# Kernel tuning notes

Hardware: AMD Instinct MI355X
Metric: run time of the kernel (lower is better)

Reference implementation:

```python
import math
import jax, jax.numpy as jnp
import numpy as np

NHEADS = 4
EPS = 1e-8


def setup_inputs() -> dict:
    key = jax.random.key(0)
    ks = jax.random.split(key, 5)
    B, C, D, H, W = 2, 64, 16, 16, 16
    dk = C // NHEADS
    x = jax.random.normal(ks[0], (B, C, D, H, W), dtype=jnp.float32)
    # xavier-uniform bound for a [nheads, dmodel, dk] tensor (torch fan_in=dmodel*dk, fan_out=nheads*dk)
    bound = math.sqrt(6.0 / (C * dk + NHEADS * dk))
    def xav(k):
        return jax.random.uniform(k, (NHEADS, C, dk), dtype=jnp.float32, minval=-bound, maxval=bound)
    return {"x": x, "wq": xav(ks[1]), "wk": xav(ks[2]), "wv": xav(ks[3]), "wo": xav(ks[4])}


def _cosine_attn(q, k, v):
    # q,k: (B,H,N,dk), v: (B,H,N,dv)
    qn = q / (jnp.linalg.norm(q, axis=-1, keepdims=True) + EPS)
    kn = k / (jnp.linalg.norm(k, axis=-1, keepdims=True) + EPS)
    scores = jnp.einsum('bhnd,bhmd->bhnm', qn, kn)  # (B,H,N,N)
    weights = jax.nn.softmax(scores, axis=-1)
    return jnp.einsum('bhnm,bhmv->bhnv', weights, v)


def reference(x, wq, wk, wv, wo):
    B, C, D, H, W = x.shape
    heads = NHEADS
    dv = C // heads
    # rearrange (B,C,D,H,W) -> (B, N, C) with N = D*H*W
    t = x.reshape(B, C, D * H * W).transpose(0, 2, 1)
    # per-kind 1/sqrt(fan_in) scaling (normalize_weight is identity here)
    wq_s = wq / math.sqrt(C)
    wk_s = wk / math.sqrt(C)
    wv_s = wv / math.sqrt(C)
    wo_s = wo / math.sqrt(heads * dv)
    q = jnp.einsum('bnc,hck->bhnk', t, wq_s)
    k = jnp.einsum('bnc,hck->bhnk', t, wk_s)
    v = jnp.einsum('bnc,hcv->bhnv', t, wv_s)
    o = _cosine_attn(q, k, v)  # (B,H,N,dv)
    y = jnp.einsum('bhnv,hcv->bnc', o, wo_s)
    return y.transpose(0, 2, 1).reshape(B, C, D, H, W)
```

## Files before the change

kernel.cpp:

```cpp
#include <hip/hip_runtime.h>
#include <math.h>

#define NHEADS 4
#define DKK 16
#define CC 64
#define BB 2
#define NN 4096
#define NBH 8
#define EPSF 1e-8f
#define KSPLIT 8
#define TILES 32
#define LOG2E 1.44269504088896340736f

typedef __attribute__((ext_vector_type(8))) short bf8;
typedef __attribute__((ext_vector_type(4))) float f4;

union Frag { bf8 v; struct { uint2 lo, hi; } p; uint4 q; };

__device__ __forceinline__ unsigned short f2bf(float f) {
    union { float f; unsigned int u; } v; v.f = f;
    unsigned int r = v.u + 0x7FFFu + ((v.u >> 16) & 1u);
    return (unsigned short)(r >> 16);
}
__device__ __forceinline__ float bf2f(unsigned short h) {
    union { unsigned int u; float f; } v; v.u = ((unsigned int)h) << 16;
    return v.f;
}

__global__ __launch_bounds__(256) void proj_kernel(
    const float* __restrict__ x, const float* __restrict__ wq,
    const float* __restrict__ wk, const float* __restrict__ wv,
    unsigned short* __restrict__ QP, unsigned short* __restrict__ KP,
    unsigned short* __restrict__ VP)
{
    __shared__ float sW[3 * CC * DKK];
    const int bh = blockIdx.x >> 6;
    const int n0 = (blockIdx.x & 63) * 64;
    const int b  = bh >> 2;
    const int h  = bh & 3;

    const int hbase = h * CC * DKK;
    for (int i = threadIdx.x; i < CC * DKK; i += 256) {
        sW[i]                = wq[hbase + i] * 0.125f;
        sW[CC * DKK + i]     = wk[hbase + i] * 0.125f;
        sW[2 * CC * DKK + i] = wv[hbase + i] * 0.125f;
    }
    __syncthreads();

    const int lane = threadIdx.x & 63;
    const int wave = threadIdx.x >> 6;
    const int n  = n0 + wave * 16 + (lane & 15);
    const int cq = lane >> 4;

    float aq[DKK] = {}, ak[DKK] = {}, av[DKK] = {};
    const float* xb = x + (size_t)b * CC * NN + n;
    for (int cc = 0; cc < 16; ++cc) {
        const int c = cq * 16 + cc;
        const float xv = xb[(size_t)c * NN];
        const float4* q4 = (const float4*)(sW + c * DKK);
        const float4* k4 = (const float4*)(sW + CC * DKK + c * DKK);
        const float4* v4 = (const float4*)(sW + 2 * CC * DKK + c * DKK);
        #pragma unroll
        for (int j = 0; j < 4; ++j) {
            float4 a = q4[j];
            aq[4*j+0] += xv * a.x; aq[4*j+1] += xv * a.y;
            aq[4*j+2] += xv * a.z; aq[4*j+3] += xv * a.w;
            float4 bk = k4[j];
            ak[4*j+0] += xv * bk.x; ak[4*j+1] += xv * bk.y;
            ak[4*j+2] += xv * bk.z; ak[4*j+3] += xv * bk.w;
            float4 cv = v4[j];
            av[4*j+0] += xv * cv.x; av[4*j+1] += xv * cv.y;
            av[4*j+2] += xv * cv.z; av[4*j+3] += xv * cv.w;
        }
    }
    #pragma unroll
    for (int i = 0; i < DKK; ++i) {
        aq[i] += __shfl_xor(aq[i], 16); aq[i] += __shfl_xor(aq[i], 32);
        ak[i] += __shfl_xor(ak[i], 16); ak[i] += __shfl_xor(ak[i], 32);
        av[i] += __shfl_xor(av[i], 16); av[i] += __shfl_xor(av[i], 32);
    }

    float sq = 0.f, sk = 0.f;
    #pragma unroll
    for (int i = 0; i < DKK; ++i) { sq += aq[i]*aq[i]; sk += ak[i]*ak[i]; }
    const float rq = LOG2E / (sqrtf(sq) + EPSF);
    const float rk = 1.0f / (sqrtf(sk) + EPSF);

    if (cq == 0) {
        __attribute__((aligned(16))) unsigned short qp[16];
        #pragma unroll
        for (int i = 0; i < DKK; ++i) qp[i] = f2bf(aq[i] * rq);
        const size_t base = ((size_t)bh * NN + n) * 16;
        ((uint4*)(QP + base))[0] = ((const uint4*)qp)[0];
        ((uint4*)(QP + base))[1] = ((const uint4*)qp)[1];
    } else if (cq == 1) {
        __attribute__((aligned(16))) unsigned short kp[16];
        #pragma unroll
        for (int i = 0; i < DKK; ++i) kp[i] = f2bf(ak[i] * rk);
        const size_t base = ((size_t)bh * NN + n) * 16;
        ((uint4*)(KP + base))[0] = ((const uint4*)kp)[0];
        ((uint4*)(KP + base))[1] = ((const uint4*)kp)[1];
    } else {
        const size_t vbase = (((size_t)bh * DKK) * 256 + (n >> 4)) * 32
                             + ((n >> 2) & 3) * 8 + (n & 3) + (cq == 2 ? 0 : 4);
        #pragma unroll
        for (int i = 0; i < DKK; ++i) {
            const float vv = av[i];
            const unsigned short hv = f2bf(vv);
            VP[vbase + (size_t)i * 256 * 32] =
                (cq == 2) ? hv : f2bf(vv - bf2f(hv));
        }
    }
}

__device__ __forceinline__ void attn_tile(
    const uint2 khi, const Frag& vc,
    const Frag* qh_, f4* oC, float* l_)
{
    const f4 zero = {0.f, 0.f, 0.f, 0.f};
    Frag kA;
    kA.p.lo = khi; kA.p.hi = make_uint2(0u, 0u);

    #pragma unroll
    for (int f = 0; f < 4; ++f) {
        f4 s = __builtin_amdgcn_mfma_f32_16x16x32_bf16(kA.v, qh_[f].v, zero, 0, 0, 0);

        const float p0 = __builtin_amdgcn_exp2f(s[0]);
        const float p1 = __builtin_amdgcn_exp2f(s[1]);
        const float p2 = __builtin_amdgcn_exp2f(s[2]);
        const float p3 = __builtin_amdgcn_exp2f(s[3]);
        l_[f] += (p0 + p1) + (p2 + p3);

        unsigned int u0, u1;
        asm("v_cvt_pk_bf16_f32 %0, %1, %2" : "=v"(u0) : "v"(p0), "v"(p1));
        asm("v_cvt_pk_bf16_f32 %0, %1, %2" : "=v"(u1) : "v"(p2), "v"(p3));
        Frag pB;
        pB.p.lo = make_uint2(u0, u1); pB.p.hi = pB.p.lo;

        oC[f] = __builtin_amdgcn_mfma_f32_16x16x32_bf16(vc.v, pB.v, oC[f], 0, 0, 0);
    }
}

__global__ __launch_bounds__(512, 4) void attn_kernel(
    const unsigned short* __restrict__ QP, const unsigned short* __restrict__ KP,
    const unsigned short* __restrict__ VP, float* __restrict__ O2T)
{
    const int bh    = blockIdx.x & 7;
    const int qg    = blockIdx.x >> 3;
    const int split = threadIdx.x >> 6;
    const int lane  = threadIdx.x & 63;
    const int g = lane >> 4;
    const int r = lane & 15;

    Frag qh_[4];
    #pragma unroll
    for (int f = 0; f < 4; ++f) {
        const uint2 qv = *(const uint2*)(QP + ((size_t)bh * NN + qg * 64 + f * 16 + r) * 16 + g * 4);
        qh_[f].p.lo = qv; qh_[f].p.hi = qv;
    }

    const int key0 = split * (NN / KSPLIT);
    const unsigned short* kp_p = KP + ((size_t)bh * NN + key0 + r) * 16 + g * 4;
    const unsigned short* vp_p = VP + (((size_t)bh * DKK + r) * 256 + (key0 >> 4)) * 32 + g * 8;

    f4 oC[4] = {{0.f,0.f,0.f,0.f},{0.f,0.f,0.f,0.f},{0.f,0.f,0.f,0.f},{0.f,0.f,0.f,0.f}};
    float l_[4] = {0.f, 0.f, 0.f, 0.f};

    uint2 k0 = *(const uint2*)kp_p;
    Frag  v0; v0.q = *(const uint4*)vp_p;
    uint2 k1 = *(const uint2*)(kp_p + 256);
    Frag  v1; v1.q = *(const uint4*)(vp_p + 32);
    kp_p += 512; vp_p += 64;

    for (int t = 0; t < TILES - 2; t += 2) {
        const uint2 kn0 = *(const uint2*)kp_p;
        Frag vn0; vn0.q = *(const uint4*)vp_p;
        attn_tile(k0, v0, qh_, oC, l_);
        const uint2 kn1 = *(const uint2*)(kp_p + 256);
        Frag vn1; vn1.q = *(const uint4*)(vp_p + 32);
        attn_tile(k1, v1, qh_, oC, l_);
        k0 = kn0; v0 = vn0; k1 = kn1; v1 = vn1;
        kp_p += 512; vp_p += 64;
    }
    attn_tile(k0, v0, qh_, oC, l_);
    attn_tile(k1, v1, qh_, oC, l_);

    #pragma unroll
    for (int f = 0; f < 4; ++f) {
        l_[f] += __shfl_xor(l_[f], 16);
        l_[f] += __shfl_xor(l_[f], 32);
    }

    __shared__ float sO[KSPLIT][4][DKK][17];
    __shared__ float sL[KSPLIT][4][17];
    #pragma unroll
    for (int f = 0; f < 4; ++f)
        #pragma unroll
        for (int i = 0; i < 4; ++i)
            sO[split][f][g * 4 + i][r] = oC[f][i];
    if (g == 0) {
        #pragma unroll
        for (int f = 0; f < 4; ++f) sL[split][f][r] = l_[f];
    }
    __syncthreads();

    const int qq  = threadIdx.x & 63;
    const int f   = qq >> 4;
    const int rr  = qq & 15;
    const int dv0 = threadIdx.x >> 6;
    const int b = bh >> 2, h = bh & 3;

    float den = 0.f;
    #pragma unroll
    for (int s = 0; s < KSPLIT; ++s) den += sL[s][f][rr];
    const float rd = 1.0f / den;

    #pragma unroll
    for (int dd = 0; dd < 2; ++dd) {
        const int dv = dv0 + dd * 8;
        float num = 0.f;
        #pragma unroll
        for (int s = 0; s < KSPLIT; ++s) num += sO[s][f][dv][rr];
        O2T[((size_t)b * CC + h * DKK + dv) * NN + qg * 64 + qq] = num * rd;
    }
}

__global__ __launch_bounds__(256) void out_kernel(
    const float* __restrict__ O2T, const float* __restrict__ wo,
    float* __restrict__ y)
{
    const int idx = blockIdx.x * 256 + threadIdx.x;
    const int n   = idx & (NN - 1);
    const int bcg = idx >> 12;
    const int cg  = bcg & 15;
    const int b   = bcg >> 4;

    const float* ob = O2T + (size_t)b * CC * NN + n;
    float acc[4] = {0.f, 0.f, 0.f, 0.f};
    #pragma unroll
    for (int h = 0; h < NHEADS; ++h)
        #pragma unroll
        for (int v = 0; v < DKK; ++v) {
            const float o = ob[(size_t)(h * DKK + v) * NN];
            #pragma unroll
            for (int c2 = 0; c2 < 4; ++c2)
                acc[c2] += o * wo[((size_t)h * CC + cg * 4 + c2) * DKK + v];
        }
    #pragma unroll
    for (int c2 = 0; c2 < 4; ++c2)
        y[((size_t)b * CC + cg * 4 + c2) * NN + n] = acc[c2] * 0.125f;
}

extern "C" void kernel_launch(void* const* d_in, const int* in_sizes, int n_in,
                              void* d_out, int out_size, void* d_ws, size_t ws_size,
                              hipStream_t stream)
{
    const float* x  = (const float*)d_in[0];
    const float* wq = (const float*)d_in[1];
    const float* wk = (const float*)d_in[2];
    const float* wv = (const float*)d_in[3];
    const float* wo = (const float*)d_in[4];
    float* y = (float*)d_out;

    const size_t QKE = (size_t)NBH * NN * 16;
    const size_t VE  = (size_t)NBH * NN * 32;
    unsigned short* QP = (unsigned short*)d_ws;
    unsigned short* KP = QP + QKE;
    unsigned short* VP = KP + QKE;
    float* O2T = (float*)(VP + VE);

    proj_kernel<<<NBH * 64, 256, 0, stream>>>(x, wq, wk, wv, QP, KP, VP);
    attn_kernel<<<NBH * 64, 512, 0, stream>>>(QP, KP, VP, O2T);
    out_kernel<<<(BB * 16 * NN) / 256, 256, 0, stream>>>(O2T, wo, y);
}
```

Before: 45.50 us.

## Drop V hi/lo bf16 split and pack 32 distinct keys per PV MFMA

V was previously stored as a bf16 hi/lo pair, and each PV MFMA spent its 32-wide K dimension on 16 keys duplicated for hi and lo. V is now stored as a single bf16 value, re-laid out so each PV MFMA consumes two 16-key score tiles at once. Each 32 keys of the key loop therefore needs one PV MFMA per query fragment instead of two, and the V buffer is half the size. In exchange, the compensated-precision V path is gone, so attention output accuracy depends on plain bf16 V.

```diff
diff --git a/kernel.cpp b/kernel.cpp
--- a/kernel.cpp
+++ b/kernel.cpp
@@ -9,7 +9,7 @@
 #define NBH 8
 #define EPSF 1e-8f
 #define KSPLIT 8
-#define TILES 32
+#define TPAIRS 16
 #define LOG2E 1.44269504088896340736f
 
 typedef __attribute__((ext_vector_type(8))) short bf8;
@@ -21,10 +21,6 @@
     union { float f; unsigned int u; } v; v.f = f;
     unsigned int r = v.u + 0x7FFFu + ((v.u >> 16) & 1u);
     return (unsigned short)(r >> 16);
-}
-__device__ __forceinline__ float bf2f(unsigned short h) {
-    union { unsigned int u; float f; } v; v.u = ((unsigned int)h) << 16;
-    return v.f;
 }
 
 __global__ __launch_bounds__(256) void proj_kernel(
@@ -101,41 +97,49 @@
         ((uint4*)(KP + base))[0] = ((const uint4*)kp)[0];
         ((uint4*)(KP + base))[1] = ((const uint4*)kp)[1];
     } else {
-        const size_t vbase = (((size_t)bh * DKK) * 256 + (n >> 4)) * 32
-                             + ((n >> 2) & 3) * 8 + (n & 3) + (cq == 2 ? 0 : 4);
-        #pragma unroll
-        for (int i = 0; i < DKK; ++i) {
-            const float vv = av[i];
-            const unsigned short hv = f2bf(vv);
-            VP[vbase + (size_t)i * 256 * 32] =
-                (cq == 2) ? hv : f2bf(vv - bf2f(hv));
+        const int vslot = ((n >> 2) & 3) * 8 + ((n >> 4) & 1) * 4 + (n & 3);
+        const int dv0 = (cq == 2) ? 0 : 8;
+        #pragma unroll
+        for (int i = 0; i < 8; ++i) {
+            const int dv = dv0 + i;
+            VP[(((size_t)bh * DKK + dv) * 128 + (n >> 5)) * 32 + vslot] = f2bf(av[dv]);
         }
     }
 }
 
-__device__ __forceinline__ void attn_tile(
-    const uint2 khi, const Frag& vc,
+__device__ __forceinline__ void attn_pair(
+    const uint2 ke, const uint2 ko, const Frag& vc,
     const Frag* qh_, f4* oC, float* l_)
 {
     const f4 zero = {0.f, 0.f, 0.f, 0.f};
-    Frag kA;
-    kA.p.lo = khi; kA.p.hi = make_uint2(0u, 0u);
+    Frag kAe, kAo;
+    kAe.p.lo = ke; kAe.p.hi = make_uint2(0u, 0u);
+    kAo.p.lo = ko; kAo.p.hi = make_uint2(0u, 0u);
 
     #pragma unroll
     for (int f = 0; f < 4; ++f) {
-        f4 s = __builtin_amdgcn_mfma_f32_16x16x32_bf16(kA.v, qh_[f].v, zero, 0, 0, 0);
-
-        const float p0 = __builtin_amdgcn_exp2f(s[0]);
-        const float p1 = __builtin_amdgcn_exp2f(s[1]);
-        const float p2 = __builtin_amdgcn_exp2f(s[2]);
-        const float p3 = __builtin_amdgcn_exp2f(s[3]);
-        l_[f] += (p0 + p1) + (p2 + p3);
-
-        unsigned int u0, u1;
-        asm("v_cvt_pk_bf16_f32 %0, %1, %2" : "=v"(u0) : "v"(p0), "v"(p1));
-        asm("v_cvt_pk_bf16_f32 %0, %1, %2" : "=v"(u1) : "v"(p2), "v"(p3));
+        f4 se = __builtin_amdgcn_mfma_f32_16x16x32_bf16(kAe.v, qh_[f].v, zero, 0, 0, 0);
+        f4 so = __builtin_amdgcn_mfma_f32_16x16x32_bf16(kAo.v, qh_[f].v, zero, 0, 0, 0);
+
+        const float pe0 = __builtin_amdgcn_exp2f(se[0]);
+        const float pe1 = __builtin_amdgcn_exp2f(se[1]);
+        const float pe2 = __builtin_amdgcn_exp2f(se[2]);
+        const float pe3 = __builtin_amdgcn_exp2f(se[3]);
+        const float po0 = __builtin_amdgcn_exp2f(so[0]);
+        const float po1 = __builtin_amdgcn_exp2f(so[1]);
+        const float po2 = __builtin_amdgcn_exp2f(so[2]);
+        const float po3 = __builtin_amdgcn_exp2f(so[3]);
+
+        l_[f] += ((pe0 + pe1) + (pe2 + pe3)) + ((po0 + po1) + (po2 + po3));
+
+        unsigned int u0, u1, u2, u3;
+        asm("v_cvt_pk_bf16_f32 %0, %1, %2" : "=v"(u0) : "v"(pe0), "v"(pe1));
+        asm("v_cvt_pk_bf16_f32 %0, %1, %2" : "=v"(u1) : "v"(pe2), "v"(pe3));
+        asm("v_cvt_pk_bf16_f32 %0, %1, %2" : "=v"(u2) : "v"(po0), "v"(po1));
+        asm("v_cvt_pk_bf16_f32 %0, %1, %2" : "=v"(u3) : "v"(po2), "v"(po3));
         Frag pB;
-        pB.p.lo = make_uint2(u0, u1); pB.p.hi = pB.p.lo;
+        pB.p.lo = make_uint2(u0, u1);
+        pB.p.hi = make_uint2(u2, u3);
 
         oC[f] = __builtin_amdgcn_mfma_f32_16x16x32_bf16(vc.v, pB.v, oC[f], 0, 0, 0);
     }
@@ -161,29 +165,34 @@
 
     const int key0 = split * (NN / KSPLIT);
     const unsigned short* kp_p = KP + ((size_t)bh * NN + key0 + r) * 16 + g * 4;
-    const unsigned short* vp_p = VP + (((size_t)bh * DKK + r) * 256 + (key0 >> 4)) * 32 + g * 8;
+    const unsigned short* vp_p = VP + (((size_t)bh * DKK + r) * 128 + (key0 >> 5)) * 32 + g * 8;
 
     f4 oC[4] = {{0.f,0.f,0.f,0.f},{0.f,0.f,0.f,0.f},{0.f,0.f,0.f,0.f},{0.f,0.f,0.f,0.f}};
     float l_[4] = {0.f, 0.f, 0.f, 0.f};
 
-    uint2 k0 = *(const uint2*)kp_p;
+    uint2 ke0 = *(const uint2*)kp_p;
+    uint2 ko0 = *(const uint2*)(kp_p + 256);
     Frag  v0; v0.q = *(const uint4*)vp_p;
-    uint2 k1 = *(const uint2*)(kp_p + 256);
+    uint2 ke1 = *(const uint2*)(kp_p + 512);
+    uint2 ko1 = *(const uint2*)(kp_p + 768);
     Frag  v1; v1.q = *(const uint4*)(vp_p + 32);
-    kp_p += 512; vp_p += 64;
-
-    for (int t = 0; t < TILES - 2; t += 2) {
-        const uint2 kn0 = *(const uint2*)kp_p;
+    kp_p += 1024; vp_p += 64;
+
+    for (int t = 0; t < TPAIRS - 2; t += 2) {
+        const uint2 kne0 = *(const uint2*)kp_p;
+        const uint2 kno0 = *(const uint2*)(kp_p + 256);
         Frag vn0; vn0.q = *(const uint4*)vp_p;
-        attn_tile(k0, v0, qh_, oC, l_);
-        const uint2 kn1 = *(const uint2*)(kp_p + 256);
+        attn_pair(ke0, ko0, v0, qh_, oC, l_);
+        const uint2 kne1 = *(const uint2*)(kp_p + 512);
+        const uint2 kno1 = *(const uint2*)(kp_p + 768);
         Frag vn1; vn1.q = *(const uint4*)(vp_p + 32);
-        attn_tile(k1, v1, qh_, oC, l_);
-        k0 = kn0; v0 = vn0; k1 = kn1; v1 = vn1;
-        kp_p += 512; vp_p += 64;
-    }
-    attn_tile(k0, v0, qh_, oC, l_);
-    attn_tile(k1, v1, qh_, oC, l_);
+        attn_pair(ke1, ko1, v1, qh_, oC, l_);
+        ke0 = kne0; ko0 = kno0; v0 = vn0;
+        ke1 = kne1; ko1 = kno1; v1 = vn1;
+        kp_p += 1024; vp_p += 64;
+    }
+    attn_pair(ke0, ko0, v0, qh_, oC, l_);
+    attn_pair(ke1, ko1, v1, qh_, oC, l_);
 
     #pragma unroll
     for (int f = 0; f < 4; ++f) {
@@ -263,7 +272,7 @@
     float* y = (float*)d_out;
 
     const size_t QKE = (size_t)NBH * NN * 16;
-    const size_t VE  = (size_t)NBH * NN * 32;
+    const size_t VE  = (size_t)NBH * DKK * 128 * 32;
     unsigned short* QP = (unsigned short*)d_ws;
     unsigned short* KP = QP + QKE;
     unsigned short* VP = KP + QKE;
```

Result: faster. 42.39 us, median of 2 (-6.8%).
